# Optimization experiments

Hardware: AMD Instinct MI355X
Metric: run time of the kernel (lower is better)

Reference implementation:

```python
import jax, jax.numpy as jnp
import numpy as np

B, L, D, DK, T = 8192, 64, 512, 64, 128
WIDE_IN = 2 * T + T * T  # 16640


def setup_inputs() -> dict:
    key = jax.random.key(0)
    ks = jax.random.split(key, 24)
    s = 0.02
    inp = {
        "mashup_tags": jax.random.uniform(ks[0], (B, T), jnp.float32),
        "target_api_tags": jax.random.uniform(ks[1], (B, T), jnp.float32),
        "cross_product_tag": jax.random.uniform(ks[2], (B, T * T), jnp.float32),
        "encoded_api_context": jax.random.normal(ks[3], (B, L, D), jnp.float32),
        "candidate_api_description_feature": jax.random.normal(ks[4], (B, D), jnp.float32),
        "mashup_description_feature": jax.random.normal(ks[5], (B, D), jnp.float32),
        "context_len": jax.random.randint(ks[6], (B,), 0, L + 1, jnp.int64 if jax.config.jax_enable_x64 else jnp.int32),
        # attention projections (torch Linear weight layout: [out, in], no bias)
        "W_K": s * jax.random.normal(ks[7], (DK, D), jnp.float32),
        "W_Q": s * jax.random.normal(ks[8], (DK, D), jnp.float32),
        # wide head
        "wide_w": s * jax.random.normal(ks[9], (1, WIDE_IN), jnp.float32),
        "wide_b": jnp.zeros((1,), jnp.float32),
        # deep MLP 1536->512->256->128->1
        "d1_w": s * jax.random.normal(ks[10], (512, 3 * D), jnp.float32),
        "d1_b": jnp.zeros((512,), jnp.float32),
        "d2_w": s * jax.random.normal(ks[11], (256, 512), jnp.float32),
        "d2_b": jnp.zeros((256,), jnp.float32),
        "d3_w": s * jax.random.normal(ks[12], (128, 256), jnp.float32),
        "d3_b": jnp.zeros((128,), jnp.float32),
        "d4_w": s * jax.random.normal(ks[13], (1, 128), jnp.float32),
        "d4_b": jnp.zeros((1,), jnp.float32),
        "wide_weight": jnp.ones((1,), jnp.float32),
        "deep_weight": jnp.ones((1,), jnp.float32),
        "bias": jnp.zeros((1,), jnp.float32),
    }
    return inp


def reference(mashup_tags, target_api_tags, cross_product_tag,
              encoded_api_context, candidate_api_description_feature,
              mashup_description_feature, context_len,
              W_K, W_Q, wide_w, wide_b,
              d1_w, d1_b, d2_w, d2_b, d3_w, d3_b, d4_w, d4_b,
              wide_weight, deep_weight, bias):
    # ---- wide branch ----
    wide_in = jnp.concatenate([mashup_tags, target_api_tags, cross_product_tag], axis=1)
    wide_out = jax.nn.sigmoid(wide_in @ wide_w.T + wide_b)  # (B,1)

    # ---- ragged attention (vectorized masked softmax replaces the Python batch loop) ----
    K = jnp.einsum("bld,kd->blk", encoded_api_context, W_K)          # (B,L,dk)
    Q = candidate_api_description_feature @ W_Q.T                     # (B,dk)
    scores = jnp.einsum("blk,bk->bl", K, Q)                           # (B,L)
    mask = jnp.arange(scores.shape[1])[None, :] < context_len[:, None]
    m = jnp.max(jnp.where(mask, scores, -1e30), axis=-1, keepdims=True)
    e = jnp.where(mask, jnp.exp(scores - m), 0.0)
    denom = jnp.sum(e, axis=-1, keepdims=True)
    probs = e / jnp.maximum(denom, 1e-30)  # rows with length==0 -> all zeros (matches torch zeros fallback)
    api_context = jnp.einsum("bl,bld->bd", probs, encoded_api_context)  # (B,512)

    # ---- deep branch ----
    deep_in = jnp.concatenate([mashup_description_feature, api_context,
                               candidate_api_description_feature], axis=1)  # (B,1536)
    h = jax.nn.relu(deep_in @ d1_w.T + d1_b)
    h = jax.nn.relu(h @ d2_w.T + d2_b)
    h = jax.nn.relu(h @ d3_w.T + d3_b)
    deep_out = h @ d4_w.T + d4_b  # (B,1)

    out = wide_weight * wide_out + deep_weight * deep_out + bias
    return jax.nn.sigmoid(out)
```

## Files before the change

kernel.cpp:

```cpp
#include <hip/hip_runtime.h>

#define Bsz 8192
#define Lctx 64
#define Ddim 512
#define DK 64
#define Ttag 128
#define RQT 2

using f32x4 = __attribute__((ext_vector_type(4))) float;
using bf16x8 = __attribute__((ext_vector_type(8))) short;

__device__ __forceinline__ float wave_sum(float v) {
#pragma unroll
    for (int m = 32; m > 0; m >>= 1) v += __shfl_xor(v, m, 64);
    return v;
}

__device__ __forceinline__ float dot4(float4 a, float4 b) {
    return a.x * b.x + a.y * b.y + a.z * b.z + a.w * b.w;
}

__device__ __forceinline__ unsigned f2bf(float f) {
    unsigned int u = __float_as_uint(f);
    u = u + 0x7fffu + ((u >> 16) & 1u);
    return u >> 16;
}
__device__ __forceinline__ unsigned pack2(float a, float b) {
    return f2bf(a) | (f2bf(b) << 16);
}
__device__ __forceinline__ float bflo(unsigned int v) { return __uint_as_float(v << 16); }
__device__ __forceinline__ float bfhi(unsigned int v) { return __uint_as_float(v & 0xffff0000u); }
__device__ __forceinline__ float bf2f(unsigned short u) { return __uint_as_float((unsigned)u << 16); }

__global__ __launch_bounds__(256) void k_f2bf3(
    const float* __restrict__ s1, unsigned short* __restrict__ d1,
    const float* __restrict__ s2, unsigned short* __restrict__ d2,
    const float* __restrict__ s3, unsigned short* __restrict__ d3)
{
    int i = blockIdx.x * 256 + threadIdx.x;
    const float* s;
    unsigned short* d;
    if (i < 196608)      { s = s1; d = d1; }
    else if (i < 229376) { i -= 196608; s = s2; d = d2; }
    else if (i < 237568) { i -= 229376; s = s3; d = d3; }
    else return;
    const float4 v = ((const float4*)s)[i];
    uint2 w;
    w.x = pack2(v.x, v.y);
    w.y = pack2(v.z, v.w);
    *(uint2*)&d[(size_t)i * 4] = w;
}

__global__ __launch_bounds__(256) void k_qtilde(
    const float* __restrict__ C, const float* __restrict__ WQ,
    const float* __restrict__ WK, float* __restrict__ qt)
{
    const int lane = threadIdx.x & 63;
    const int gw = blockIdx.x * 4 + (threadIdx.x >> 6);
    const int b0 = gw * RQT;

    float4 c0[RQT], c1[RQT];
#pragma unroll
    for (int r = 0; r < RQT; ++r) {
        const float4* row = (const float4*)(C + (size_t)(b0 + r) * Ddim);
        c0[r] = row[lane];
        c1[r] = row[64 + lane];
    }
    float tv[RQT];
#pragma unroll
    for (int r = 0; r < RQT; ++r) tv[r] = 0.f;
    for (int k = 0; k < DK; ++k) {
        const float4* wrow = (const float4*)(WQ + (size_t)k * Ddim);
        const float4 w0 = wrow[lane];
        const float4 w1 = wrow[64 + lane];
#pragma unroll
        for (int r = 0; r < RQT; ++r) {
            float p = dot4(c0[r], w0) + dot4(c1[r], w1);
            p = wave_sum(p);
            if (lane == k) tv[r] = p;
        }
    }
    float4 a0[RQT], a1[RQT];
#pragma unroll
    for (int r = 0; r < RQT; ++r) {
        a0[r] = make_float4(0.f, 0.f, 0.f, 0.f);
        a1[r] = make_float4(0.f, 0.f, 0.f, 0.f);
    }
    for (int k = 0; k < DK; ++k) {
        const float4* wrow = (const float4*)(WK + (size_t)k * Ddim);
        const float4 w0 = wrow[lane];
        const float4 w1 = wrow[64 + lane];
#pragma unroll
        for (int r = 0; r < RQT; ++r) {
            const float tk = __shfl(tv[r], k, 64);
            a0[r].x += tk * w0.x; a0[r].y += tk * w0.y;
            a0[r].z += tk * w0.z; a0[r].w += tk * w0.w;
            a1[r].x += tk * w1.x; a1[r].y += tk * w1.y;
            a1[r].z += tk * w1.z; a1[r].w += tk * w1.w;
        }
    }
#pragma unroll
    for (int r = 0; r < RQT; ++r) {
        float4* orow = (float4*)(qt + (size_t)(b0 + r) * Ddim);
        orow[lane] = a0[r];
        orow[64 + lane] = a1[r];
    }
}

__global__ __launch_bounds__(256, 2) void k_attn_wide(
    const float* __restrict__ X, const float* __restrict__ qt,
    const int* __restrict__ clen, const float* __restrict__ mdesc,
    const float* __restrict__ cand,
    const float* __restrict__ mt, const float* __restrict__ tt,
    const float* __restrict__ cp, const float* __restrict__ ww,
    const float* __restrict__ wb,
    unsigned short* __restrict__ din, float* __restrict__ wl)
{
    __shared__ float sl[Lctx];
    __shared__ float pl[Lctx];
    __shared__ float part[4][Ddim];
    __shared__ float red[4];

    const int b = blockIdx.x;
    const int tid = threadIdx.x;
    const int wave = tid >> 6, lane = tid & 63;
    const int len = clen[b];
    const int nrows = min(16, max(0, len - wave * 16));

    const float4* qrow = (const float4*)(qt + (size_t)b * Ddim);
    const float4 q0 = qrow[lane];
    const float4 q1 = qrow[64 + lane];
    const float4* xb = (const float4*)(X + (size_t)b * Lctx * Ddim);

    uint2 pk[16][2];
    float sc[16];

#pragma unroll
    for (int g = 0; g < 4; ++g) {
        if (g * 4 < nrows) {
            float4 t0[4], t1[4];
#pragma unroll
            for (int i = 0; i < 4; ++i) {
                if (g * 4 + i < nrows) {
                    const int l = wave * 16 + g * 4 + i;
                    t0[i] = xb[l * 128 + lane];
                    t1[i] = xb[l * 128 + 64 + lane];
                }
            }
#pragma unroll
            for (int i = 0; i < 4; ++i) {
                if (g * 4 + i < nrows) {
                    const int r = g * 4 + i;
                    sc[r] = dot4(t0[i], q0) + dot4(t1[i], q1);
                    pk[r][0].x = pack2(t0[i].x, t0[i].y);
                    pk[r][0].y = pack2(t0[i].z, t0[i].w);
                    pk[r][1].x = pack2(t1[i].x, t1[i].y);
                    pk[r][1].y = pack2(t1[i].z, t1[i].w);
                }
            }
        }
    }
#pragma unroll
    for (int r = 0; r < 16; ++r)
        if (r < nrows) sc[r] = wave_sum(sc[r]);
    if (lane == 0) {
#pragma unroll
        for (int r = 0; r < 16; ++r)
            if (r < nrows) sl[wave * 16 + r] = sc[r];
    }

    float wacc = 0.f;
    if (tid < 64) {
        float4 v;
        if (tid < 32) v = ((const float4*)(mt + (size_t)b * Ttag))[tid];
        else          v = ((const float4*)(tt + (size_t)b * Ttag))[tid - 32];
        wacc += dot4(v, ((const float4*)ww)[tid]);
    }
    {
        const float4* cp4 = (const float4*)(cp + (size_t)b * (Ttag * Ttag));
        const float4* ww4 = (const float4*)(ww + 2 * Ttag);
#pragma unroll 4
        for (int i = tid; i < (Ttag * Ttag) / 4; i += 256)
            wacc += dot4(cp4[i], ww4[i]);
    }
    wacc = wave_sum(wacc);
    if (lane == 0) red[wave] = wacc;

    __syncthreads();

    float m = -1e30f;
    for (int l = 0; l < len; ++l) m = fmaxf(m, sl[l]);
    float denom = 0.f;
    for (int l = 0; l < len; ++l) denom += __expf(sl[l] - m);
    const float rden = 1.f / fmaxf(denom, 1e-30f);
    if (tid < Lctx) pl[tid] = (tid < len) ? __expf(sl[tid] - m) * rden : 0.f;
    __syncthreads();

    float4 a0 = make_float4(0.f, 0.f, 0.f, 0.f);
    float4 a1 = make_float4(0.f, 0.f, 0.f, 0.f);
#pragma unroll
    for (int r = 0; r < 16; ++r) {
        if (r < nrows) {
            const float p = pl[wave * 16 + r];
            a0.x += p * bflo(pk[r][0].x); a0.y += p * bfhi(pk[r][0].x);
            a0.z += p * bflo(pk[r][0].y); a0.w += p * bfhi(pk[r][0].y);
            a1.x += p * bflo(pk[r][1].x); a1.y += p * bfhi(pk[r][1].x);
            a1.z += p * bflo(pk[r][1].y); a1.w += p * bfhi(pk[r][1].y);
        }
    }
    *(float4*)&part[wave][lane * 4] = a0;
    *(float4*)&part[wave][256 + lane * 4] = a1;
    __syncthreads();

    unsigned short* dr = din + (size_t)b * 1536;
    {
        const int d0 = tid * 2;
        const float2 s0 = *(const float2*)&part[0][d0];
        const float2 s1 = *(const float2*)&part[1][d0];
        const float2 s2 = *(const float2*)&part[2][d0];
        const float2 s3 = *(const float2*)&part[3][d0];
        const float vx = s0.x + s1.x + s2.x + s3.x;
        const float vy = s0.y + s1.y + s2.y + s3.y;
        *(unsigned*)&dr[512 + d0] = pack2(vx, vy);
    }
    {
        const float4 v = (tid < 128)
            ? ((const float4*)(mdesc + (size_t)b * Ddim))[tid]
            : ((const float4*)(cand + (size_t)b * Ddim))[tid - 128];
        uint2 w;
        w.x = pack2(v.x, v.y);
        w.y = pack2(v.z, v.w);
        const int off = (tid < 128) ? tid * 4 : 1024 + (tid - 128) * 4;
        *(uint2*)&dr[off] = w;
    }
    if (tid == 0) wl[b] = red[0] + red[1] + red[2] + red[3] + wb[0];
}

__global__ __launch_bounds__(256) void k_gemm_bf16(
    const unsigned short* __restrict__ A, const unsigned short* __restrict__ W,
    const float* __restrict__ bias, unsigned short* __restrict__ C,
    const int K, const int N, const int relu)
{
    __shared__ unsigned short As[128][72];
    __shared__ unsigned short Bs[128][72];
    const int tid = threadIdx.x;
    const int wave = tid >> 6, lane = tid & 63;
    const int wm = wave >> 1, wn = wave & 1;
    const size_t m0 = (size_t)blockIdx.x * 128;
    const size_t n0 = (size_t)blockIdx.y * 128;

    f32x4 acc[4][4];
#pragma unroll
    for (int i = 0; i < 4; ++i)
#pragma unroll
        for (int j = 0; j < 4; ++j) acc[i][j] = (f32x4){0.f, 0.f, 0.f, 0.f};

    uint4 pa[4], pb[4];
    auto loadA = [&](int k0) {
#pragma unroll
        for (int j = 0; j < 4; ++j) {
            const int i = tid + j * 256;
            const int row = i >> 3, c8 = (i & 7) * 8;
            pa[j] = *(const uint4*)(A + (m0 + row) * (size_t)K + k0 + c8);
        }
    };
    auto loadB = [&](int k0) {
#pragma unroll
        for (int j = 0; j < 4; ++j) {
            const int i = tid + j * 256;
            const int row = i >> 3, c8 = (i & 7) * 8;
            pb[j] = *(const uint4*)(W + (n0 + row) * (size_t)K + k0 + c8);
        }
    };

    loadA(0);
    loadB(0);
    for (int k0 = 0; k0 < K; k0 += 64) {
        __syncthreads();
#pragma unroll
        for (int j = 0; j < 4; ++j) {
            const int i = tid + j * 256;
            const int row = i >> 3, c8 = (i & 7) * 8;
            *(uint4*)&As[row][c8] = pa[j];
            *(uint4*)&Bs[row][c8] = pb[j];
        }
        __syncthreads();
        if (k0 + 64 < K) { loadA(k0 + 64); loadB(k0 + 64); }
#pragma unroll
        for (int kk = 0; kk < 2; ++kk) {
            const int krow = kk * 32 + (lane >> 4) * 8;
            bf16x8 af[4], bfr[4];
#pragma unroll
            for (int mm = 0; mm < 4; ++mm)
                af[mm] = *(const bf16x8*)&As[wm * 64 + mm * 16 + (lane & 15)][krow];
#pragma unroll
            for (int nn = 0; nn < 4; ++nn)
                bfr[nn] = *(const bf16x8*)&Bs[wn * 64 + nn * 16 + (lane & 15)][krow];
#pragma unroll
            for (int mm = 0; mm < 4; ++mm)
#pragma unroll
                for (int nn = 0; nn < 4; ++nn)
                    acc[mm][nn] = __builtin_amdgcn_mfma_f32_16x16x32_bf16(
                        af[mm], bfr[nn], acc[mm][nn], 0, 0, 0);
        }
    }

#pragma unroll
    for (int nn = 0; nn < 4; ++nn) {
        const int col = (int)n0 + wn * 64 + nn * 16 + (lane & 15);
        const float bv = bias[col];
#pragma unroll
        for (int mm = 0; mm < 4; ++mm) {
#pragma unroll
            for (int r = 0; r < 4; ++r) {
                const size_t row = m0 + wm * 64 + mm * 16 + (lane >> 4) * 4 + r;
                float v = acc[mm][nn][r] + bv;
                if (relu) v = fmaxf(v, 0.f);
                C[row * N + col] = (unsigned short)f2bf(v);
            }
        }
    }
}

__global__ __launch_bounds__(256) void k_final(
    const unsigned short* __restrict__ h3, const float* __restrict__ d4w,
    const float* __restrict__ d4b, const float* __restrict__ wl,
    const float* __restrict__ wwt, const float* __restrict__ dwt,
    const float* __restrict__ bs, float* __restrict__ out)
{
    const int lane = threadIdx.x & 63;
    const int b = blockIdx.x * 4 + (threadIdx.x >> 6);
    const unsigned short* hr = h3 + (size_t)b * 128;
    float v = bf2f(hr[lane]) * d4w[lane] + bf2f(hr[64 + lane]) * d4w[64 + lane];
    v = wave_sum(v);
    if (lane == 0) {
        const float deep = v + d4b[0];
        const float wo = 1.f / (1.f + __expf(-wl[b]));
        const float z = wwt[0] * wo + dwt[0] * deep + bs[0];
        out[b] = 1.f / (1.f + __expf(-z));
    }
}

extern "C" void kernel_launch(void* const* d_in, const int* in_sizes, int n_in,
                              void* d_out, int out_size, void* d_ws, size_t ws_size,
                              hipStream_t stream)
{
    const float* mt    = (const float*)d_in[0];
    const float* tt    = (const float*)d_in[1];
    const float* cp    = (const float*)d_in[2];
    const float* X     = (const float*)d_in[3];
    const float* cand  = (const float*)d_in[4];
    const float* mdesc = (const float*)d_in[5];
    const int*   clen  = (const int*)d_in[6];
    const float* WK    = (const float*)d_in[7];
    const float* WQ    = (const float*)d_in[8];
    const float* ww    = (const float*)d_in[9];
    const float* wb    = (const float*)d_in[10];
    const float* d1w   = (const float*)d_in[11];
    const float* d1b   = (const float*)d_in[12];
    const float* d2w   = (const float*)d_in[13];
    const float* d2b   = (const float*)d_in[14];
    const float* d3w   = (const float*)d_in[15];
    const float* d3b   = (const float*)d_in[16];
    const float* d4w   = (const float*)d_in[17];
    const float* d4b   = (const float*)d_in[18];
    const float* wwt   = (const float*)d_in[19];
    const float* dwt   = (const float*)d_in[20];
    const float* bs    = (const float*)d_in[21];
    float* out = (float*)d_out;

    char* w = (char*)d_ws;
    unsigned short* din = (unsigned short*)w;            w += (size_t)Bsz * 1536 * 2;
    float* qt           = (float*)w;                     w += (size_t)Bsz * 512 * 4;
    unsigned short* h1  = (unsigned short*)w;            w += (size_t)Bsz * 512 * 2;
    unsigned short* h2  = (unsigned short*)w;            w += (size_t)Bsz * 256 * 2;
    unsigned short* h3  = (unsigned short*)w;            w += (size_t)Bsz * 128 * 2;
    float* wl           = (float*)w;                     w += (size_t)Bsz * 4;
    unsigned short* w1b = (unsigned short*)w;            w += (size_t)512 * 1536 * 2;
    unsigned short* w2b = (unsigned short*)w;            w += (size_t)256 * 512 * 2;
    unsigned short* w3b = (unsigned short*)w;            w += (size_t)128 * 256 * 2;

    hipLaunchKernelGGL(k_f2bf3, dim3(928), dim3(256), 0, stream,
                       d1w, w1b, d2w, w2b, d3w, w3b);
    hipLaunchKernelGGL(k_qtilde, dim3(Bsz / (RQT * 4)), dim3(256), 0, stream,
                       cand, WQ, WK, qt);
    hipLaunchKernelGGL(k_attn_wide, dim3(Bsz), dim3(256), 0, stream,
                       X, qt, clen, mdesc, cand, mt, tt, cp, ww, wb, din, wl);
    hipLaunchKernelGGL(k_gemm_bf16, dim3(64, 4), dim3(256), 0, stream,
                       din, w1b, d1b, h1, 1536, 512, 1);
    hipLaunchKernelGGL(k_gemm_bf16, dim3(64, 2), dim3(256), 0, stream,
                       h1, w2b, d2b, h2, 512, 256, 1);
    hipLaunchKernelGGL(k_gemm_bf16, dim3(64, 1), dim3(256), 0, stream,
                       h2, w3b, d3b, h3, 256, 128, 1);
    hipLaunchKernelGGL(k_final, dim3(Bsz / 4), dim3(256), 0, stream,
                       h3, d4w, d4b, wl, wwt, dwt, bs, out);
}
```

Before: 443.2 us.

## Use 512-thread blocks with 8 rows per wave in attention-wide kernel

The attention/wide kernel now runs 8 waves per block instead of 4, so each wave handles 8 context rows rather than 16. All 8 row loads are issued up front, with the row index clamped so out-of-range slots reload a valid row. The serial per-thread softmax over scores is replaced by a single-wave shuffle reduction. The idea is more memory-level parallelism and lower register pressure per wave for the bandwidth-bound context read and the cross-tag dot product, at the cost of a larger block, more shared memory for partials, and narrower output stores.

Result: faster. 407.1 us (-8.1%).

```diff
diff --git a/kernel.cpp b/kernel.cpp
--- a/kernel.cpp
+++ b/kernel.cpp
@@ -107,7 +107,7 @@
     }
 }
 
-__global__ __launch_bounds__(256, 2) void k_attn_wide(
+__global__ __launch_bounds__(512, 2) void k_attn_wide(
     const float* __restrict__ X, const float* __restrict__ qt,
     const int* __restrict__ clen, const float* __restrict__ mdesc,
     const float* __restrict__ cand,
@@ -118,55 +118,49 @@
 {
     __shared__ float sl[Lctx];
     __shared__ float pl[Lctx];
-    __shared__ float part[4][Ddim];
-    __shared__ float red[4];
+    __shared__ float part[8][Ddim];
+    __shared__ float red[8];
 
     const int b = blockIdx.x;
     const int tid = threadIdx.x;
     const int wave = tid >> 6, lane = tid & 63;
     const int len = clen[b];
-    const int nrows = min(16, max(0, len - wave * 16));
+    const int nrows = min(8, max(0, len - wave * 8));
 
     const float4* qrow = (const float4*)(qt + (size_t)b * Ddim);
     const float4 q0 = qrow[lane];
     const float4 q1 = qrow[64 + lane];
     const float4* xb = (const float4*)(X + (size_t)b * Lctx * Ddim);
 
-    uint2 pk[16][2];
-    float sc[16];
-
-#pragma unroll
-    for (int g = 0; g < 4; ++g) {
-        if (g * 4 < nrows) {
-            float4 t0[4], t1[4];
-#pragma unroll
-            for (int i = 0; i < 4; ++i) {
-                if (g * 4 + i < nrows) {
-                    const int l = wave * 16 + g * 4 + i;
-                    t0[i] = xb[l * 128 + lane];
-                    t1[i] = xb[l * 128 + 64 + lane];
-                }
+    uint2 pk[8][2];
+    float sc[8];
+
+    if (nrows > 0) {
+        float4 t0[8], t1[8];
+#pragma unroll
+        for (int r = 0; r < 8; ++r) {
+            const int l = wave * 8 + min(r, nrows - 1);
+            t0[r] = xb[l * 128 + lane];
+            t1[r] = xb[l * 128 + 64 + lane];
+        }
+#pragma unroll
+        for (int r = 0; r < 8; ++r) {
+            if (r < nrows) {
+                sc[r] = dot4(t0[r], q0) + dot4(t1[r], q1);
+                pk[r][0].x = pack2(t0[r].x, t0[r].y);
+                pk[r][0].y = pack2(t0[r].z, t0[r].w);
+                pk[r][1].x = pack2(t1[r].x, t1[r].y);
+                pk[r][1].y = pack2(t1[r].z, t1[r].w);
             }
-#pragma unroll
-            for (int i = 0; i < 4; ++i) {
-                if (g * 4 + i < nrows) {
-                    const int r = g * 4 + i;
-                    sc[r] = dot4(t0[i], q0) + dot4(t1[i], q1);
-                    pk[r][0].x = pack2(t0[i].x, t0[i].y);
-                    pk[r][0].y = pack2(t0[i].z, t0[i].w);
-                    pk[r][1].x = pack2(t1[i].x, t1[i].y);
-                    pk[r][1].y = pack2(t1[i].z, t1[i].w);
-                }
-            }
-        }
-    }
-#pragma unroll
-    for (int r = 0; r < 16; ++r)
-        if (r < nrows) sc[r] = wave_sum(sc[r]);
-    if (lane == 0) {
-#pragma unroll
-        for (int r = 0; r < 16; ++r)
-            if (r < nrows) sl[wave * 16 + r] = sc[r];
+        }
+#pragma unroll
+        for (int r = 0; r < 8; ++r)
+            if (r < nrows) sc[r] = wave_sum(sc[r]);
+        if (lane == 0) {
+#pragma unroll
+            for (int r = 0; r < 8; ++r)
+                if (r < nrows) sl[wave * 8 + r] = sc[r];
+        }
     }
 
     float wacc = 0.f;
@@ -180,7 +174,7 @@
         const float4* cp4 = (const float4*)(cp + (size_t)b * (Ttag * Ttag));
         const float4* ww4 = (const float4*)(ww + 2 * Ttag);
 #pragma unroll 4
-        for (int i = tid; i < (Ttag * Ttag) / 4; i += 256)
+        for (int i = tid; i < (Ttag * Ttag) / 4; i += 512)
             wacc += dot4(cp4[i], ww4[i]);
     }
     wacc = wave_sum(wacc);
@@ -188,20 +182,24 @@
 
     __syncthreads();
 
-    float m = -1e30f;
-    for (int l = 0; l < len; ++l) m = fmaxf(m, sl[l]);
-    float denom = 0.f;
-    for (int l = 0; l < len; ++l) denom += __expf(sl[l] - m);
-    const float rden = 1.f / fmaxf(denom, 1e-30f);
-    if (tid < Lctx) pl[tid] = (tid < len) ? __expf(sl[tid] - m) * rden : 0.f;
+    if (wave == 0) {
+        const float s = (lane < len) ? sl[lane] : -1e30f;
+        float m = s;
+#pragma unroll
+        for (int msk = 32; msk > 0; msk >>= 1)
+            m = fmaxf(m, __shfl_xor(m, msk, 64));
+        const float e = (lane < len) ? __expf(s - m) : 0.f;
+        const float d = wave_sum(e);
+        pl[lane] = e * (1.f / fmaxf(d, 1e-30f));
+    }
     __syncthreads();
 
     float4 a0 = make_float4(0.f, 0.f, 0.f, 0.f);
     float4 a1 = make_float4(0.f, 0.f, 0.f, 0.f);
 #pragma unroll
-    for (int r = 0; r < 16; ++r) {
+    for (int r = 0; r < 8; ++r) {
         if (r < nrows) {
-            const float p = pl[wave * 16 + r];
+            const float p = pl[wave * 8 + r];
             a0.x += p * bflo(pk[r][0].x); a0.y += p * bfhi(pk[r][0].x);
             a0.z += p * bflo(pk[r][0].y); a0.w += p * bfhi(pk[r][0].y);
             a1.x += p * bflo(pk[r][1].x); a1.y += p * bfhi(pk[r][1].x);
@@ -214,16 +212,12 @@
 
     unsigned short* dr = din + (size_t)b * 1536;
     {
-        const int d0 = tid * 2;
-        const float2 s0 = *(const float2*)&part[0][d0];
-        const float2 s1 = *(const float2*)&part[1][d0];
-        const float2 s2 = *(const float2*)&part[2][d0];
-        const float2 s3 = *(const float2*)&part[3][d0];
-        const float vx = s0.x + s1.x + s2.x + s3.x;
-        const float vy = s0.y + s1.y + s2.y + s3.y;
-        *(unsigned*)&dr[512 + d0] = pack2(vx, vy);
-    }
-    {
+        float v = 0.f;
+#pragma unroll
+        for (int w8 = 0; w8 < 8; ++w8) v += part[w8][tid];
+        dr[512 + tid] = (unsigned short)f2bf(v);
+    }
+    if (tid < 256) {
         const float4 v = (tid < 128)
             ? ((const float4*)(mdesc + (size_t)b * Ddim))[tid]
             : ((const float4*)(cand + (size_t)b * Ddim))[tid - 128];
@@ -233,7 +227,9 @@
         const int off = (tid < 128) ? tid * 4 : 1024 + (tid - 128) * 4;
         *(uint2*)&dr[off] = w;
     }
-    if (tid == 0) wl[b] = red[0] + red[1] + red[2] + red[3] + wb[0];
+    if (tid == 0)
+        wl[b] = red[0] + red[1] + red[2] + red[3] +
+                red[4] + red[5] + red[6] + red[7] + wb[0];
 }
 
 __global__ __launch_bounds__(256) void k_gemm_bf16(
@@ -384,7 +380,7 @@
                        d1w, w1b, d2w, w2b, d3w, w3b);
     hipLaunchKernelGGL(k_qtilde, dim3(Bsz / (RQT * 4)), dim3(256), 0, stream,
                        cand, WQ, WK, qt);
-    hipLaunchKernelGGL(k_attn_wide, dim3(Bsz), dim3(256), 0, stream,
+    hipLaunchKernelGGL(k_attn_wide, dim3(Bsz), dim3(512), 0, stream,
                        X, qt, clen, mdesc, cand, mt, tt, cp, ww, wb, din, wl);
     hipLaunchKernelGGL(k_gemm_bf16, dim3(64, 4), dim3(256), 0, stream,
                        din, w1b, d1b, h1, 1536, 512, 1);
```

## Use online softmax in attention to drop register row cache and raise occupancy

Applied to the files above, without the earlier changes.

The attention kernel now has each wave take interleaved context rows and fold them into an online-softmax running max and weighted sum. The raw rows no longer have to be held in registers as packed bf16 until the global softmax is known. The per-wave partial sums are rescaled by the global max and denominator in the final reduction, which removes one block barrier and the probability array. Launch bounds go from 2 to 8 blocks per CU, so more blocks can overlap their memory traffic. The cost is extra exp and rescale arithmetic per row pair, and fp32 accumulation replaces the earlier bf16-rounded rows.

Measured after the change: 406.8 us. 8.2% less time.

```diff
diff --git a/kernel.cpp b/kernel.cpp
--- a/kernel.cpp
+++ b/kernel.cpp
@@ -16,6 +16,12 @@
     return v;
 }
 
+__device__ __forceinline__ float wave_max(float v) {
+#pragma unroll
+    for (int m = 32; m > 0; m >>= 1) v = fmaxf(v, __shfl_xor(v, m, 64));
+    return v;
+}
+
 __device__ __forceinline__ float dot4(float4 a, float4 b) {
     return a.x * b.x + a.y * b.y + a.z * b.z + a.w * b.w;
 }
@@ -28,8 +34,6 @@
 __device__ __forceinline__ unsigned pack2(float a, float b) {
     return f2bf(a) | (f2bf(b) << 16);
 }
-__device__ __forceinline__ float bflo(unsigned int v) { return __uint_as_float(v << 16); }
-__device__ __forceinline__ float bfhi(unsigned int v) { return __uint_as_float(v & 0xffff0000u); }
 __device__ __forceinline__ float bf2f(unsigned short u) { return __uint_as_float((unsigned)u << 16); }
 
 __global__ __launch_bounds__(256) void k_f2bf3(
@@ -107,7 +111,7 @@
     }
 }
 
-__global__ __launch_bounds__(256, 2) void k_attn_wide(
+__global__ __launch_bounds__(256, 8) void k_attn_wide(
     const float* __restrict__ X, const float* __restrict__ qt,
     const int* __restrict__ clen, const float* __restrict__ mdesc,
     const float* __restrict__ cand,
@@ -117,57 +121,62 @@
     unsigned short* __restrict__ din, float* __restrict__ wl)
 {
     __shared__ float sl[Lctx];
-    __shared__ float pl[Lctx];
     __shared__ float part[4][Ddim];
+    __shared__ float Mw[4];
     __shared__ float red[4];
+    __shared__ float MD[2];
 
     const int b = blockIdx.x;
     const int tid = threadIdx.x;
     const int wave = tid >> 6, lane = tid & 63;
     const int len = clen[b];
-    const int nrows = min(16, max(0, len - wave * 16));
-
-    const float4* qrow = (const float4*)(qt + (size_t)b * Ddim);
-    const float4 q0 = qrow[lane];
-    const float4 q1 = qrow[64 + lane];
+    const int nrw = (len > wave) ? ((len - wave + 3) >> 2) : 0;
+
     const float4* xb = (const float4*)(X + (size_t)b * Lctx * Ddim);
 
-    uint2 pk[16][2];
-    float sc[16];
-
-#pragma unroll
-    for (int g = 0; g < 4; ++g) {
-        if (g * 4 < nrows) {
-            float4 t0[4], t1[4];
-#pragma unroll
-            for (int i = 0; i < 4; ++i) {
-                if (g * 4 + i < nrows) {
-                    const int l = wave * 16 + g * 4 + i;
-                    t0[i] = xb[l * 128 + lane];
-                    t1[i] = xb[l * 128 + 64 + lane];
-                }
+    float4 y0 = make_float4(0.f, 0.f, 0.f, 0.f);
+    float4 y1 = make_float4(0.f, 0.f, 0.f, 0.f);
+    float mw = -1e30f;
+
+    if (nrw > 0) {
+        const float4* qrow = (const float4*)(qt + (size_t)b * Ddim);
+        const float4 q0 = qrow[lane];
+        const float4 q1 = qrow[64 + lane];
+        for (int k = 0; k < nrw; k += 2) {
+            const int l0 = wave + k * 4;
+            const int l1 = wave + min(k + 1, nrw - 1) * 4;
+            const float4 a0 = xb[l0 * 128 + lane];
+            const float4 a1 = xb[l0 * 128 + 64 + lane];
+            const float4 c0 = xb[l1 * 128 + lane];
+            const float4 c1 = xb[l1 * 128 + 64 + lane];
+            float s0 = dot4(a0, q0) + dot4(a1, q1);
+            float s1 = dot4(c0, q0) + dot4(c1, q1);
+            s0 = wave_sum(s0);
+            s1 = wave_sum(s1);
+            const bool has1 = (k + 1 < nrw);
+            if (lane == 0) {
+                sl[l0] = s0;
+                if (has1) sl[l1] = s1;
             }
-#pragma unroll
-            for (int i = 0; i < 4; ++i) {
-                if (g * 4 + i < nrows) {
-                    const int r = g * 4 + i;
-                    sc[r] = dot4(t0[i], q0) + dot4(t1[i], q1);
-                    pk[r][0].x = pack2(t0[i].x, t0[i].y);
-                    pk[r][0].y = pack2(t0[i].z, t0[i].w);
-                    pk[r][1].x = pack2(t1[i].x, t1[i].y);
-                    pk[r][1].y = pack2(t1[i].z, t1[i].w);
-                }
-            }
-        }
-    }
-#pragma unroll
-    for (int r = 0; r < 16; ++r)
-        if (r < nrows) sc[r] = wave_sum(sc[r]);
-    if (lane == 0) {
-#pragma unroll
-        for (int r = 0; r < 16; ++r)
-            if (r < nrows) sl[wave * 16 + r] = sc[r];
-    }
+            const float pm = has1 ? fmaxf(s0, s1) : s0;
+            const float mn = fmaxf(mw, pm);
+            const float scale = __expf(mw - mn);
+            const float e0 = __expf(s0 - mn);
+            const float e1 = has1 ? __expf(s1 - mn) : 0.f;
+            y0.x = y0.x * scale + e0 * a0.x + e1 * c0.x;
+            y0.y = y0.y * scale + e0 * a0.y + e1 * c0.y;
+            y0.z = y0.z * scale + e0 * a0.z + e1 * c0.z;
+            y0.w = y0.w * scale + e0 * a0.w + e1 * c0.w;
+            y1.x = y1.x * scale + e0 * a1.x + e1 * c1.x;
+            y1.y = y1.y * scale + e0 * a1.y + e1 * c1.y;
+            y1.z = y1.z * scale + e0 * a1.z + e1 * c1.z;
+            y1.w = y1.w * scale + e0 * a1.w + e1 * c1.w;
+            mw = mn;
+        }
+    }
+    *(float4*)&part[wave][lane * 4] = y0;
+    *(float4*)&part[wave][256 + lane * 4] = y1;
+    if (lane == 0) Mw[wave] = mw;
 
     float wacc = 0.f;
     if (tid < 64) {
@@ -179,57 +188,52 @@
     {
         const float4* cp4 = (const float4*)(cp + (size_t)b * (Ttag * Ttag));
         const float4* ww4 = (const float4*)(ww + 2 * Ttag);
-#pragma unroll 4
+#pragma unroll 2
         for (int i = tid; i < (Ttag * Ttag) / 4; i += 256)
             wacc += dot4(cp4[i], ww4[i]);
     }
     wacc = wave_sum(wacc);
     if (lane == 0) red[wave] = wacc;
 
+    const float4 mv = (tid < 128)
+        ? ((const float4*)(mdesc + (size_t)b * Ddim))[tid]
+        : ((const float4*)(cand + (size_t)b * Ddim))[tid - 128];
+
     __syncthreads();
 
-    float m = -1e30f;
-    for (int l = 0; l < len; ++l) m = fmaxf(m, sl[l]);
-    float denom = 0.f;
-    for (int l = 0; l < len; ++l) denom += __expf(sl[l] - m);
-    const float rden = 1.f / fmaxf(denom, 1e-30f);
-    if (tid < Lctx) pl[tid] = (tid < len) ? __expf(sl[tid] - m) * rden : 0.f;
+    if (wave == 0) {
+        const float s = (lane < len) ? sl[lane] : -1e30f;
+        const float m = wave_max(s);
+        const float e = (lane < len) ? __expf(s - m) : 0.f;
+        const float d = wave_sum(e);
+        if (lane == 0) {
+            MD[0] = m;
+            MD[1] = 1.f / fmaxf(d, 1e-30f);
+        }
+    }
     __syncthreads();
 
-    float4 a0 = make_float4(0.f, 0.f, 0.f, 0.f);
-    float4 a1 = make_float4(0.f, 0.f, 0.f, 0.f);
-#pragma unroll
-    for (int r = 0; r < 16; ++r) {
-        if (r < nrows) {
-            const float p = pl[wave * 16 + r];
-            a0.x += p * bflo(pk[r][0].x); a0.y += p * bfhi(pk[r][0].x);
-            a0.z += p * bflo(pk[r][0].y); a0.w += p * bfhi(pk[r][0].y);
-            a1.x += p * bflo(pk[r][1].x); a1.y += p * bfhi(pk[r][1].x);
-            a1.z += p * bflo(pk[r][1].y); a1.w += p * bfhi(pk[r][1].y);
-        }
-    }
-    *(float4*)&part[wave][lane * 4] = a0;
-    *(float4*)&part[wave][256 + lane * 4] = a1;
-    __syncthreads();
+    const float Mg = MD[0], rD = MD[1];
+    const float f0 = __expf(Mw[0] - Mg) * rD;
+    const float f1 = __expf(Mw[1] - Mg) * rD;
+    const float f2 = __expf(Mw[2] - Mg) * rD;
+    const float f3 = __expf(Mw[3] - Mg) * rD;
 
     unsigned short* dr = din + (size_t)b * 1536;
     {
         const int d0 = tid * 2;
-        const float2 s0 = *(const float2*)&part[0][d0];
-        const float2 s1 = *(const float2*)&part[1][d0];
-        const float2 s2 = *(const float2*)&part[2][d0];
-        const float2 s3 = *(const float2*)&part[3][d0];
-        const float vx = s0.x + s1.x + s2.x + s3.x;
-        const float vy = s0.y + s1.y + s2.y + s3.y;
+        const float2 p0 = *(const float2*)&part[0][d0];
+        const float2 p1 = *(const float2*)&part[1][d0];
+        const float2 p2 = *(const float2*)&part[2][d0];
+        const float2 p3 = *(const float2*)&part[3][d0];
+        const float vx = p0.x * f0 + p1.x * f1 + p2.x * f2 + p3.x * f3;
+        const float vy = p0.y * f0 + p1.y * f1 + p2.y * f2 + p3.y * f3;
         *(unsigned*)&dr[512 + d0] = pack2(vx, vy);
     }
     {
-        const float4 v = (tid < 128)
-            ? ((const float4*)(mdesc + (size_t)b * Ddim))[tid]
-            : ((const float4*)(cand + (size_t)b * Ddim))[tid - 128];
         uint2 w;
-        w.x = pack2(v.x, v.y);
-        w.y = pack2(v.z, v.w);
+        w.x = pack2(mv.x, mv.y);
+        w.y = pack2(mv.z, mv.w);
         const int off = (tid < 128) ? tid * 4 : 1024 + (tid - 128) * 4;
         *(uint2*)&dr[off] = w;
     }
```
